# Performance work log

Measured on AMD Instinct MI355X. Metric: run time of the kernel, lower is better.

The kernel has to match this reference:

```python
import jax, jax.numpy as jnp
import numpy as np
import math

B, S, D, H = 2, 2048, 1024, 16
DK = D // H


def setup_inputs() -> dict:
    key = jax.random.key(0)
    ks = jax.random.split(key, 12)
    std = 1.0 / math.sqrt(D)
    inp = {
        "q": jax.random.normal(ks[0], (B, S, D), jnp.float32),
        "k": jax.random.normal(ks[1], (B, S, D), jnp.float32),
        "v": jax.random.normal(ks[2], (B, S, D), jnp.float32),
        # causal mask, broadcast over batch and heads
        "mask": jnp.tril(jnp.ones((S, S), jnp.int32))[None, None, :, :],
        "wq": jax.random.normal(ks[3], (D, D), jnp.float32) * std,
        "bq": jax.random.normal(ks[4], (D,), jnp.float32) * std,
        "wk": jax.random.normal(ks[5], (D, D), jnp.float32) * std,
        "bk": jax.random.normal(ks[6], (D,), jnp.float32) * std,
        "wv": jax.random.normal(ks[7], (D, D), jnp.float32) * std,
        "bv": jax.random.normal(ks[8], (D,), jnp.float32) * std,
        "wo": jax.random.normal(ks[9], (D, D), jnp.float32) * std,
        "bo": jax.random.normal(ks[10], (D,), jnp.float32) * std,
    }
    return inp


def _split_heads(x):
    # [B,S,D] -> [B,H,S,DK]
    b, s, _ = x.shape
    return x.reshape(b, s, H, DK).transpose(0, 2, 1, 3)


def reference(q, k, v, mask, wq, bq, wk, bk, wv, bv, wo, bo):
    # nn.Linear: y = x @ W^T + b
    query = _split_heads(q @ wq.T + bq)
    key_h = _split_heads(k @ wk.T + bk)
    value = _split_heads(v @ wv.T + bv)

    scale = 1.0 / math.sqrt(DK)
    scores = jnp.einsum("bhqd,bhkd->bhqk", query, key_h) * scale  # [B,H,S,S]
    scores = jnp.where(mask == 0, jnp.float32(-1e9), scores)
    attn = jax.nn.softmax(scores, axis=-1)  # dropout p=0.0 -> identity

    x = jnp.einsum("bhqk,bhkd->bhqd", attn, value)  # [B,H,S,DK]
    x = x.transpose(0, 2, 1, 3).reshape(q.shape[0], -1, H * DK)  # [B,S,D]
    return x @ wo.T + bo
```

## Files before the change

kernel.cpp:

```cpp
#include <hip/hip_runtime.h>

#define B_SZ    2
#define S_LEN   2048
#define D_MODEL 1024
#define H_NUM   16
#define DK_H    64
#define M_ROWS  (B_SZ * S_LEN)

typedef __attribute__((ext_vector_type(8))) short  short8;
typedef __attribute__((ext_vector_type(4))) short  short4v;
typedef __attribute__((ext_vector_type(4))) float  floatx4;

__device__ __forceinline__ short f2b(float f) {
    union { float f; unsigned u; } x; x.f = f;
    unsigned u = x.u + 0x7fffu + ((x.u >> 16) & 1u);
    return (short)(u >> 16);
}
__device__ __forceinline__ short f2b_t(float f) {
    union { float f; unsigned u; } x; x.f = f;
    return (short)(x.u >> 16);
}

typedef __attribute__((address_space(1))) const unsigned int gu32;
typedef __attribute__((address_space(3))) unsigned int       lu32;
__device__ __forceinline__ void gload_lds16(const short* g, short* l) {
    __builtin_amdgcn_global_load_lds((gu32*)g, (lu32*)l, 16, 0, 0);
}

#define QSCALE 0.18033688011112042f
#define SM_SHIFT 12.0f

__global__ void cvt_all_kernel(const float* __restrict__ xq, const float* __restrict__ xk,
                               const float* __restrict__ xv, const float* __restrict__ wq,
                               const float* __restrict__ wk, const float* __restrict__ wv,
                               const float* __restrict__ wo,
                               short* __restrict__ oxq, short* __restrict__ oxk,
                               short* __restrict__ oxv, short* __restrict__ owq,
                               short* __restrict__ owk, short* __restrict__ owv,
                               short* __restrict__ owo)
{
    const int y = blockIdx.y;
    const float* in;
    short* out;
    switch (y) {
        case 0: in = xq; out = oxq; break;
        case 1: in = xk; out = oxk; break;
        case 2: in = xv; out = oxv; break;
        case 3: in = wq; out = owq; break;
        case 4: in = wk; out = owk; break;
        case 5: in = wv; out = owv; break;
        default: in = wo; out = owo; break;
    }
    const int npass = (y < 3) ? 4 : 1;
    int base = blockIdx.x * 1024 + threadIdx.x * 4;
    for (int p = 0; p < npass; ++p) {
        int i = base + p * 1048576;
        float4 v = *(const float4*)(in + i);
        short4v r;
        r[0] = f2b(v.x); r[1] = f2b(v.y); r[2] = f2b(v.z); r[3] = f2b(v.w);
        *(short4v*)(out + i) = r;
    }
}

__global__ __launch_bounds__(256)
void gemm_qkv_kernel(const short* __restrict__ xq, const short* __restrict__ xk,
                     const short* __restrict__ xv,
                     const short* __restrict__ wq, const short* __restrict__ wk,
                     const short* __restrict__ wv,
                     const float* __restrict__ bq, const float* __restrict__ bk,
                     const float* __restrict__ bv,
                     short* __restrict__ Qp, short* __restrict__ Kp, short* __restrict__ Vt)
{
    __shared__ short sa[128 * 32];
    __shared__ short sb[128 * 32];

    const int which = blockIdx.y >> 3;
    const short* A    = (which == 0) ? xq : (which == 1) ? xk : xv;
    const short* W    = (which == 0) ? wq : (which == 1) ? wk : wv;
    const float* bias = (which == 0) ? bq : (which == 1) ? bk : bv;
    const float scale = (which == 0) ? QSCALE : 1.0f;

    const int nb = (blockIdx.y & 7) * 128;
    const int m0 = blockIdx.x * 128;
    const int t = threadIdx.x, wave = t >> 6, lane = t & 63;
    const int quad = lane >> 4, l16 = lane & 15;
    const int wm = (wave & 1) * 64, wn = (wave >> 1) * 64;

    const int r0 = t >> 2, cs = t & 3;
    const int c0 = cs ^ ((r0 >> 1) & 3);
    const short* Ab0 = A + (size_t)(m0 + r0) * D_MODEL + c0 * 8;
    const short* Ab1 = Ab0 + (size_t)64 * D_MODEL;
    const short* Bb0 = W + (size_t)(nb + r0) * D_MODEL + c0 * 8;
    const short* Bb1 = Bb0 + (size_t)64 * D_MODEL;
    short* sa0 = sa + t * 8;  short* sa1 = sa + 2048 + t * 8;
    short* sb0 = sb + t * 8;  short* sb1 = sb + 2048 + t * 8;

    int a_off[4], b_off[4];
#pragma unroll
    for (int i = 0; i < 4; ++i) {
        int ar = wm + i * 16 + l16;
        a_off[i] = ar * 32 + ((quad ^ ((ar >> 1) & 3)) * 8);
        int br = wn + i * 16 + l16;
        b_off[i] = br * 32 + ((quad ^ ((br >> 1) & 3)) * 8);
    }

    floatx4 acc[4][4] = {};
    for (int k0 = 0; k0 < D_MODEL; k0 += 32) {
        __syncthreads();
        gload_lds16(Ab0 + k0, sa0);
        gload_lds16(Ab1 + k0, sa1);
        gload_lds16(Bb0 + k0, sb0);
        gload_lds16(Bb1 + k0, sb1);
        __syncthreads();
        short8 af[4], bf[4];
#pragma unroll
        for (int i = 0; i < 4; ++i) af[i] = *(const short8*)(sa + a_off[i]);
#pragma unroll
        for (int i = 0; i < 4; ++i) bf[i] = *(const short8*)(sb + b_off[i]);
#pragma unroll
        for (int mt = 0; mt < 4; ++mt)
#pragma unroll
            for (int nt = 0; nt < 4; ++nt)
                acc[mt][nt] = __builtin_amdgcn_mfma_f32_16x16x32_bf16(af[mt], bf[nt], acc[mt][nt], 0, 0, 0);
    }

#pragma unroll
    for (int nt = 0; nt < 4; ++nt) {
        int ncol = nb + wn + nt * 16 + l16;
        int h = ncol >> 6, dk = ncol & 63;
        float bv_ = bias[ncol];
#pragma unroll
        for (int mt = 0; mt < 4; ++mt) {
            int mrow0 = m0 + wm + mt * 16 + quad * 4;
            int bb = mrow0 >> 11, s0 = mrow0 & (S_LEN - 1);
            if (which < 2) {
                short* Out = (which == 0) ? Qp : Kp;
#pragma unroll
                for (int r = 0; r < 4; ++r) {
                    float v = (acc[mt][nt][r] + bv_) * scale;
                    Out[(((size_t)bb * H_NUM + h) * S_LEN + (s0 + r)) * DK_H + dk] = f2b(v);
                }
            } else {
                short4v pk;
#pragma unroll
                for (int r = 0; r < 4; ++r) pk[r] = f2b(acc[mt][nt][r] + bv_);
                *(short4v*)(&Vt[(((size_t)bb * H_NUM + h) * DK_H + dk) * S_LEN + s0]) = pk;
            }
        }
    }
}

__global__ __launch_bounds__(512, 2)
void attn_kernel(const short* __restrict__ Qp, const short* __restrict__ Kp,
                 const short* __restrict__ Vt, short* __restrict__ Xa)
{
    __shared__ short pl[8][16 * 72];

    const int c = (int)(blockIdx.x + 8 * blockIdx.y);
    const int bh = c & 31;
    const int pairtile = c >> 5;
    const int t = threadIdx.x, wave = t >> 6, lane = t & 63;
    const int quad = lane >> 4, l16 = lane & 15;
    const int tile = (wave < 4) ? pairtile : (15 - pairtile);
    const int wv = wave & 3;

    const short* Qb  = Qp + (size_t)bh * S_LEN * DK_H;
    const short* Kb  = Kp + (size_t)bh * S_LEN * DK_H;
    const short* Vtb = Vt + (size_t)bh * DK_H * S_LEN;

    const int q0 = tile * 128 + wv * 32;
    const int ktimax = (q0 + 31) >> 6;

    short8 qf[2][2];
#pragma unroll
    for (int g = 0; g < 2; ++g)
#pragma unroll
        for (int ks = 0; ks < 2; ++ks)
            qf[g][ks] = *(const short8*)(Qb + (size_t)(q0 + g * 16 + l16) * DK_H + ks * 32 + quad * 8);

    short8 bl = {};
    if (l16 == 0) {
#pragma unroll
        for (int j = 0; j < 8; ++j) bl[j] = (short)0x3F80;
    }

    floatx4 o[2][4] = {};
    floatx4 ol[2] = {};
    short* plw = &pl[wave][0];

    short8 bk0[4][2], bk1[4][2];
#pragma unroll
    for (int nt = 0; nt < 4; ++nt)
#pragma unroll
        for (int ks = 0; ks < 2; ++ks)
            bk0[nt][ks] = *(const short8*)(Kb + (size_t)(nt * 16 + l16) * DK_H + ks * 32 + quad * 8);

    auto step = [&](int kti, short8 (&bkc)[4][2], short8 (&bkn)[4][2]) {
        const int kbase = kti * 64;

        short8 bv[4][2];
#pragma unroll
        for (int nt = 0; nt < 4; ++nt)
#pragma unroll
            for (int ks = 0; ks < 2; ++ks)
                bv[nt][ks] = *(const short8*)(Vtb + (size_t)(nt * 16 + l16) * S_LEN + kbase + ks * 32 + quad * 8);

        floatx4 sc[2][4] = {};
#pragma unroll
        for (int g = 0; g < 2; ++g)
#pragma unroll
            for (int nt = 0; nt < 4; ++nt)
#pragma unroll
                for (int ks = 0; ks < 2; ++ks)
                    sc[g][nt] = __builtin_amdgcn_mfma_f32_16x16x32_bf16(qf[g][ks], bkc[nt][ks], sc[g][nt], 0, 0, 0);

        if (kti < ktimax) {
#pragma unroll
            for (int nt = 0; nt < 4; ++nt)
#pragma unroll
                for (int ks = 0; ks < 2; ++ks)
                    bkn[nt][ks] = *(const short8*)(Kb + (size_t)(kbase + 64 + nt * 16 + l16) * DK_H + ks * 32 + quad * 8);
        }

        const bool diag = (kti == ktimax);

#pragma unroll
        for (int g = 0; g < 2; ++g) {
            const int qg = q0 + g * 16 + quad * 4;
            if (diag) {
#pragma unroll
                for (int nt = 0; nt < 4; ++nt) {
                    int key = kbase + nt * 16 + l16;
#pragma unroll
                    for (int r = 0; r < 4; ++r)
                        if (key > qg + r) sc[g][nt][r] = -1e30f;
                }
            }

#pragma unroll
            for (int nt = 0; nt < 4; ++nt)
#pragma unroll
                for (int r = 0; r < 4; ++r)
                    plw[(quad * 4 + r) * 72 + nt * 16 + l16] = f2b_t(exp2f(sc[g][nt][r] - SM_SHIFT));

            short8 ap0 = *(const short8*)(plw + l16 * 72 + quad * 8);
            short8 ap1 = *(const short8*)(plw + l16 * 72 + 32 + quad * 8);

#pragma unroll
            for (int nt = 0; nt < 4; ++nt) {
                o[g][nt] = __builtin_amdgcn_mfma_f32_16x16x32_bf16(ap0, bv[nt][0], o[g][nt], 0, 0, 0);
                o[g][nt] = __builtin_amdgcn_mfma_f32_16x16x32_bf16(ap1, bv[nt][1], o[g][nt], 0, 0, 0);
            }
            ol[g] = __builtin_amdgcn_mfma_f32_16x16x32_bf16(ap0, bl, ol[g], 0, 0, 0);
            ol[g] = __builtin_amdgcn_mfma_f32_16x16x32_bf16(ap1, bl, ol[g], 0, 0, 0);
        }
    };

    for (int kti = 0; kti <= ktimax; ) {
        step(kti, bk0, bk1);
        ++kti;
        if (kti <= ktimax) {
            step(kti, bk1, bk0);
            ++kti;
        }
    }

    const int b_ = bh >> 4, h = bh & 15;
#pragma unroll
    for (int g = 0; g < 2; ++g) {
#pragma unroll
        for (int r = 0; r < 4; ++r) {
            float lsum = __shfl(ol[g][r], (lane & 48));
            float rinv = 1.0f / lsum;
            int srow = q0 + g * 16 + quad * 4 + r;
#pragma unroll
            for (int nt = 0; nt < 4; ++nt) {
                int col = h * 64 + nt * 16 + l16;
                Xa[((size_t)b_ * S_LEN + srow) * D_MODEL + col] = f2b(o[g][nt][r] * rinv);
            }
        }
    }
}

__global__ __launch_bounds__(256)
void gemm_out_kernel(const short* __restrict__ A, const short* __restrict__ W,
                     const float* __restrict__ bias, float* __restrict__ out)
{
    __shared__ short sa[128 * 32];
    __shared__ short sb[128 * 32];

    const int nb = blockIdx.y * 128;
    const int m0 = blockIdx.x * 128;
    const int t = threadIdx.x, wave = t >> 6, lane = t & 63;
    const int quad = lane >> 4, l16 = lane & 15;
    const int wm = (wave & 1) * 64, wn = (wave >> 1) * 64;

    const int r0 = t >> 2, cs = t & 3;
    const int c0 = cs ^ ((r0 >> 1) & 3);
    const short* Ab0 = A + (size_t)(m0 + r0) * D_MODEL + c0 * 8;
    const short* Ab1 = Ab0 + (size_t)64 * D_MODEL;
    const short* Bb0 = W + (size_t)(nb + r0) * D_MODEL + c0 * 8;
    const short* Bb1 = Bb0 + (size_t)64 * D_MODEL;
    short* sa0 = sa + t * 8;  short* sa1 = sa + 2048 + t * 8;
    short* sb0 = sb + t * 8;  short* sb1 = sb + 2048 + t * 8;

    int a_off[4], b_off[4];
#pragma unroll
    for (int i = 0; i < 4; ++i) {
        int ar = wm + i * 16 + l16;
        a_off[i] = ar * 32 + ((quad ^ ((ar >> 1) & 3)) * 8);
        int br = wn + i * 16 + l16;
        b_off[i] = br * 32 + ((quad ^ ((br >> 1) & 3)) * 8);
    }

    floatx4 acc[4][4] = {};
    for (int k0 = 0; k0 < D_MODEL; k0 += 32) {
        __syncthreads();
        gload_lds16(Ab0 + k0, sa0);
        gload_lds16(Ab1 + k0, sa1);
        gload_lds16(Bb0 + k0, sb0);
        gload_lds16(Bb1 + k0, sb1);
        __syncthreads();
        short8 af[4], bf[4];
#pragma unroll
    for (int i = 0; i < 4; ++i) af[i] = *(const short8*)(sa + a_off[i]);
#pragma unroll
        for (int i = 0; i < 4; ++i) bf[i] = *(const short8*)(sb + b_off[i]);
#pragma unroll
        for (int mt = 0; mt < 4; ++mt)
#pragma unroll
            for (int nt = 0; nt < 4; ++nt)
                acc[mt][nt] = __builtin_amdgcn_mfma_f32_16x16x32_bf16(af[mt], bf[nt], acc[mt][nt], 0, 0, 0);
    }

#pragma unroll
    for (int nt = 0; nt < 4; ++nt) {
        int ncol = nb + wn + nt * 16 + l16;
        float bv_ = bias[ncol];
#pragma unroll
        for (int mt = 0; mt < 4; ++mt) {
            int mrow0 = m0 + wm + mt * 16 + quad * 4;
#pragma unroll
            for (int r = 0; r < 4; ++r)
                out[(size_t)(mrow0 + r) * D_MODEL + ncol] = acc[mt][nt][r] + bv_;
        }
    }
}

extern "C" void kernel_launch(void* const* d_in, const int* in_sizes, int n_in,
                              void* d_out, int out_size, void* d_ws, size_t ws_size,
                              hipStream_t stream)
{
    (void)in_sizes; (void)n_in; (void)out_size; (void)ws_size;
    const float* q  = (const float*)d_in[0];
    const float* k  = (const float*)d_in[1];
    const float* v  = (const float*)d_in[2];
    const float* wq = (const float*)d_in[4];
    const float* bq = (const float*)d_in[5];
    const float* wk = (const float*)d_in[6];
    const float* bk = (const float*)d_in[7];
    const float* wv = (const float*)d_in[8];
    const float* bv = (const float*)d_in[9];
    const float* wo = (const float*)d_in[10];
    const float* bo = (const float*)d_in[11];
    float* out = (float*)d_out;

    const size_t XE = (size_t)M_ROWS * D_MODEL;
    const size_t WE = (size_t)D_MODEL * D_MODEL;
    short* ws_  = (short*)d_ws;
    short* xq_b = ws_;
    short* xk_b = xq_b + XE;
    short* xv_b = xk_b + XE;
    short* wq_b = xv_b + XE;
    short* wk_b = wq_b + WE;
    short* wv_b = wk_b + WE;
    short* wo_b = wv_b + WE;
    short* Qp   = wo_b + WE;
    short* Kp   = Qp + XE;
    short* Vt   = Kp + XE;
    short* Xa   = xq_b;

    dim3 blk(256);
    cvt_all_kernel<<<dim3(1024, 7), blk, 0, stream>>>(
        q, k, v, wq, wk, wv, wo, xq_b, xk_b, xv_b, wq_b, wk_b, wv_b, wo_b);

    gemm_qkv_kernel<<<dim3(M_ROWS / 128, 24), blk, 0, stream>>>(
        xq_b, xk_b, xv_b, wq_b, wk_b, wv_b, bq, bk, bv, Qp, Kp, Vt);

    attn_kernel<<<dim3(8, B_SZ * H_NUM), dim3(512), 0, stream>>>(Qp, Kp, Vt, Xa);

    gemm_out_kernel<<<dim3(M_ROWS / 128, D_MODEL / 128), blk, 0, stream>>>(Xa, wo_b, bo, out);
}
```

Baseline: 261.2 us.

## Split attention rows across 16 waves and permute V layout for packed P stores

The attention kernel now launches 1024-thread blocks where each wave owns 16 query rows instead of 32, doubling wave-level parallelism and halving per-wave register state. The V projection epilogue writes Vt with a permuted key order within each 64-key block. That lets the probability tile be written to LDS as packed 64-bit stores of four bf16 values, replacing sixteen scalar stores, while keeping the P×V product consistent. The trade-off is that each K/V fragment loaded from global memory now serves only 16 query rows, so K/V load traffic per query doubles. The Vt writes also become scattered scalar stores instead of 4-wide vectors.

Measured after the change: 384.2 us. 1.47x slower.

```diff
diff --git a/kernel.cpp b/kernel.cpp
--- a/kernel.cpp
+++ b/kernel.cpp
@@ -15,10 +15,6 @@
     union { float f; unsigned u; } x; x.f = f;
     unsigned u = x.u + 0x7fffu + ((x.u >> 16) & 1u);
     return (short)(u >> 16);
-}
-__device__ __forceinline__ short f2b_t(float f) {
-    union { float f; unsigned u; } x; x.f = f;
-    return (short)(x.u >> 16);
 }
 
 typedef __attribute__((address_space(1))) const unsigned int gu32;
@@ -141,42 +137,43 @@
                     Out[(((size_t)bb * H_NUM + h) * S_LEN + (s0 + r)) * DK_H + dk] = f2b(v);
                 }
             } else {
-                short4v pk;
-#pragma unroll
-                for (int r = 0; r < 4; ++r) pk[r] = f2b(acc[mt][nt][r] + bv_);
-                *(short4v*)(&Vt[(((size_t)bb * H_NUM + h) * DK_H + dk) * S_LEN + s0]) = pk;
+                int Sb = s0 & ~63, sb0_ = s0 & 63;
+                size_t rowbase = (((size_t)bb * H_NUM + h) * DK_H + dk) * S_LEN + Sb;
+#pragma unroll
+                for (int r = 0; r < 4; ++r) {
+                    int cc = sb0_ + r;
+                    Vt[rowbase + ((cc & 15) * 4 + (cc >> 4))] = f2b(acc[mt][nt][r] + bv_);
+                }
             }
         }
     }
 }
 
-__global__ __launch_bounds__(512, 2)
+__global__ __launch_bounds__(1024, 4)
 void attn_kernel(const short* __restrict__ Qp, const short* __restrict__ Kp,
                  const short* __restrict__ Vt, short* __restrict__ Xa)
 {
-    __shared__ short pl[8][16 * 72];
+    __shared__ short pl[16][16 * 72];
 
     const int c = (int)(blockIdx.x + 8 * blockIdx.y);
     const int bh = c & 31;
     const int pairtile = c >> 5;
     const int t = threadIdx.x, wave = t >> 6, lane = t & 63;
     const int quad = lane >> 4, l16 = lane & 15;
-    const int tile = (wave < 4) ? pairtile : (15 - pairtile);
-    const int wv = wave & 3;
+    const int tile = (wave < 8) ? pairtile : (15 - pairtile);
+    const int wv = wave & 7;
 
     const short* Qb  = Qp + (size_t)bh * S_LEN * DK_H;
     const short* Kb  = Kp + (size_t)bh * S_LEN * DK_H;
     const short* Vtb = Vt + (size_t)bh * DK_H * S_LEN;
 
-    const int q0 = tile * 128 + wv * 32;
-    const int ktimax = (q0 + 31) >> 6;
-
-    short8 qf[2][2];
-#pragma unroll
-    for (int g = 0; g < 2; ++g)
-#pragma unroll
-        for (int ks = 0; ks < 2; ++ks)
-            qf[g][ks] = *(const short8*)(Qb + (size_t)(q0 + g * 16 + l16) * DK_H + ks * 32 + quad * 8);
+    const int q0 = tile * 128 + wv * 16;
+    const int ktimax = (q0 + 15) >> 6;
+
+    short8 qf[2];
+#pragma unroll
+    for (int ks = 0; ks < 2; ++ks)
+        qf[ks] = *(const short8*)(Qb + (size_t)(q0 + l16) * DK_H + ks * 32 + quad * 8);
 
     short8 bl = {};
     if (l16 == 0) {
@@ -184,9 +181,10 @@
         for (int j = 0; j < 8; ++j) bl[j] = (short)0x3F80;
     }
 
-    floatx4 o[2][4] = {};
-    floatx4 ol[2] = {};
+    floatx4 o[4] = {};
+    floatx4 ol = {};
     short* plw = &pl[wave][0];
+    const int qg = q0 + quad * 4;
 
     short8 bk0[4][2], bk1[4][2];
 #pragma unroll
@@ -205,14 +203,12 @@
             for (int ks = 0; ks < 2; ++ks)
                 bv[nt][ks] = *(const short8*)(Vtb + (size_t)(nt * 16 + l16) * S_LEN + kbase + ks * 32 + quad * 8);
 
-        floatx4 sc[2][4] = {};
-#pragma unroll
-        for (int g = 0; g < 2; ++g)
-#pragma unroll
-            for (int nt = 0; nt < 4; ++nt)
-#pragma unroll
-                for (int ks = 0; ks < 2; ++ks)
-                    sc[g][nt] = __builtin_amdgcn_mfma_f32_16x16x32_bf16(qf[g][ks], bkc[nt][ks], sc[g][nt], 0, 0, 0);
+        floatx4 sc[4] = {};
+#pragma unroll
+        for (int nt = 0; nt < 4; ++nt)
+#pragma unroll
+            for (int ks = 0; ks < 2; ++ks)
+                sc[nt] = __builtin_amdgcn_mfma_f32_16x16x32_bf16(qf[ks], bkc[nt][ks], sc[nt], 0, 0, 0);
 
         if (kti < ktimax) {
 #pragma unroll
@@ -222,38 +218,39 @@
                     bkn[nt][ks] = *(const short8*)(Kb + (size_t)(kbase + 64 + nt * 16 + l16) * DK_H + ks * 32 + quad * 8);
         }
 
-        const bool diag = (kti == ktimax);
-
-#pragma unroll
-        for (int g = 0; g < 2; ++g) {
-            const int qg = q0 + g * 16 + quad * 4;
-            if (diag) {
-#pragma unroll
-                for (int nt = 0; nt < 4; ++nt) {
-                    int key = kbase + nt * 16 + l16;
-#pragma unroll
-                    for (int r = 0; r < 4; ++r)
-                        if (key > qg + r) sc[g][nt][r] = -1e30f;
-                }
+        if (kti == ktimax) {
+#pragma unroll
+            for (int nt = 0; nt < 4; ++nt) {
+                int key = kbase + nt * 16 + l16;
+#pragma unroll
+                for (int r = 0; r < 4; ++r)
+                    if (key > qg + r) sc[nt][r] = -1e30f;
             }
-
-#pragma unroll
-            for (int nt = 0; nt < 4; ++nt)
-#pragma unroll
-                for (int r = 0; r < 4; ++r)
-                    plw[(quad * 4 + r) * 72 + nt * 16 + l16] = f2b_t(exp2f(sc[g][nt][r] - SM_SHIFT));
-
-            short8 ap0 = *(const short8*)(plw + l16 * 72 + quad * 8);
-            short8 ap1 = *(const short8*)(plw + l16 * 72 + 32 + quad * 8);
-
-#pragma unroll
-            for (int nt = 0; nt < 4; ++nt) {
-                o[g][nt] = __builtin_amdgcn_mfma_f32_16x16x32_bf16(ap0, bv[nt][0], o[g][nt], 0, 0, 0);
-                o[g][nt] = __builtin_amdgcn_mfma_f32_16x16x32_bf16(ap1, bv[nt][1], o[g][nt], 0, 0, 0);
-            }
-            ol[g] = __builtin_amdgcn_mfma_f32_16x16x32_bf16(ap0, bl, ol[g], 0, 0, 0);
-            ol[g] = __builtin_amdgcn_mfma_f32_16x16x32_bf16(ap1, bl, ol[g], 0, 0, 0);
-        }
+        }
+
+#pragma unroll
+        for (int r = 0; r < 4; ++r) {
+            union { float f; unsigned u; } a0, a1, a2, a3;
+            a0.f = exp2f(sc[0][r] - SM_SHIFT);
+            a1.f = exp2f(sc[1][r] - SM_SHIFT);
+            a2.f = exp2f(sc[2][r] - SM_SHIFT);
+            a3.f = exp2f(sc[3][r] - SM_SHIFT);
+            uint2 d;
+            d.x = (a1.u & 0xffff0000u) | (a0.u >> 16);
+            d.y = (a3.u & 0xffff0000u) | (a2.u >> 16);
+            *(uint2*)(plw + (quad * 4 + r) * 72 + l16 * 4) = d;
+        }
+
+        short8 ap0 = *(const short8*)(plw + l16 * 72 + quad * 8);
+        short8 ap1 = *(const short8*)(plw + l16 * 72 + 32 + quad * 8);
+
+#pragma unroll
+        for (int nt = 0; nt < 4; ++nt) {
+            o[nt] = __builtin_amdgcn_mfma_f32_16x16x32_bf16(ap0, bv[nt][0], o[nt], 0, 0, 0);
+            o[nt] = __builtin_amdgcn_mfma_f32_16x16x32_bf16(ap1, bv[nt][1], o[nt], 0, 0, 0);
+        }
+        ol = __builtin_amdgcn_mfma_f32_16x16x32_bf16(ap0, bl, ol, 0, 0, 0);
+        ol = __builtin_amdgcn_mfma_f32_16x16x32_bf16(ap1, bl, ol, 0, 0, 0);
     };
 
     for (int kti = 0; kti <= ktimax; ) {
@@ -267,17 +264,14 @@
 
     const int b_ = bh >> 4, h = bh & 15;
 #pragma unroll
-    for (int g = 0; g < 2; ++g) {
-#pragma unroll
-        for (int r = 0; r < 4; ++r) {
-            float lsum = __shfl(ol[g][r], (lane & 48));
-            float rinv = 1.0f / lsum;
-            int srow = q0 + g * 16 + quad * 4 + r;
-#pragma unroll
-            for (int nt = 0; nt < 4; ++nt) {
-                int col = h * 64 + nt * 16 + l16;
-                Xa[((size_t)b_ * S_LEN + srow) * D_MODEL + col] = f2b(o[g][nt][r] * rinv);
-            }
+    for (int r = 0; r < 4; ++r) {
+        float lsum = __shfl(ol[r], (lane & 48));
+        float rinv = 1.0f / lsum;
+        int srow = qg + r;
+#pragma unroll
+        for (int nt = 0; nt < 4; ++nt) {
+            int col = h * 64 + nt * 16 + l16;
+            Xa[((size_t)b_ * S_LEN + srow) * D_MODEL + col] = f2b(o[nt][r] * rinv);
         }
     }
 }
@@ -323,7 +317,7 @@
         __syncthreads();
         short8 af[4], bf[4];
 #pragma unroll
-    for (int i = 0; i < 4; ++i) af[i] = *(const short8*)(sa + a_off[i]);
+        for (int i = 0; i < 4; ++i) af[i] = *(const short8*)(sa + a_off[i]);
 #pragma unroll
         for (int i = 0; i < 4; ++i) bf[i] = *(const short8*)(sb + b_off[i]);
 #pragma unroll
@@ -387,7 +381,7 @@
     gemm_qkv_kernel<<<dim3(M_ROWS / 128, 24), blk, 0, stream>>>(
         xq_b, xk_b, xv_b, wq_b, wk_b, wv_b, bq, bk, bv, Qp, Kp, Vt);
 
-    attn_kernel<<<dim3(8, B_SZ * H_NUM), dim3(512), 0, stream>>>(Qp, Kp, Vt, Xa);
+    attn_kernel<<<dim3(8, B_SZ * H_NUM), dim3(1024), 0, stream>>>(Qp, Kp, Vt, Xa);
 
     gemm_out_kernel<<<dim3(M_ROWS / 128, D_MODEL / 128), blk, 0, stream>>>(Xa, wo_b, bo, out);
 }
```
